# Optimization experiments

Measured on AMD Instinct MI355X. Metric: run time of the kernel, lower is better.

## Reference

```python
import jax, jax.numpy as jnp
import numpy as np

D_MODEL = 1024
NHEAD = 16
HEAD_DIM = D_MODEL // NHEAD
WINDOW = 256


def setup_inputs() -> dict:
    key = jax.random.key(0)
    kx, kq, kk, kv, ko = jax.random.split(key, 5)
    B, S = 2, 2048
    scale = 1.0 / np.sqrt(D_MODEL)
    x = jax.random.normal(kx, (B, S, D_MODEL), dtype=jnp.float32)
    Wq = jax.random.normal(kq, (D_MODEL, D_MODEL), dtype=jnp.float32) * scale
    Wk = jax.random.normal(kk, (D_MODEL, D_MODEL), dtype=jnp.float32) * scale
    Wv = jax.random.normal(kv, (D_MODEL, D_MODEL), dtype=jnp.float32) * scale
    Wo = jax.random.normal(ko, (D_MODEL, D_MODEL), dtype=jnp.float32) * scale
    return {"x": x, "Wq": Wq, "Wk": Wk, "Wv": Wv, "Wo": Wo}


def _sliding_window_mask(seq_len):
    # additive mask: 0 where (q - window + 1) <= k <= q, -inf elsewhere
    pos = jnp.arange(seq_len)
    qpos = pos[:, None]
    kpos = pos[None, :]
    valid = (kpos >= qpos - WINDOW + 1) & (kpos <= qpos)
    return jnp.where(valid, 0.0, -jnp.inf).astype(jnp.float32)


def reference(x, Wq, Wk, Wv, Wo):
    B, S, D = x.shape
    # projections (nn.Linear: x @ W.T; weights here stored as [out,in] equiv -> use x @ W.T)
    q = jnp.einsum('bsd,ed->bse', x, Wq)
    k = jnp.einsum('bsd,ed->bse', x, Wk)
    v = jnp.einsum('bsd,ed->bse', x, Wv)
    q = q.reshape(B, S, NHEAD, HEAD_DIM).transpose(0, 2, 1, 3)  # [B,H,S,Dh]
    k = k.reshape(B, S, NHEAD, HEAD_DIM).transpose(0, 2, 1, 3)
    v = v.reshape(B, S, NHEAD, HEAD_DIM).transpose(0, 2, 1, 3)
    mask = _sliding_window_mask(S)  # [S,S]
    scale = 1.0 / np.sqrt(HEAD_DIM)
    scores = jnp.einsum('bhqd,bhkd->bhqk', q, k) * scale + mask
    attn = jax.nn.softmax(scores, axis=-1)
    out = jnp.einsum('bhqk,bhkd->bhqd', attn, v)  # [B,H,S,Dh]
    out = out.transpose(0, 2, 1, 3).reshape(B, S, D)
    return jnp.einsum('bsd,ed->bse', out, Wo)
```

## Files before the change

kernel.cpp:

```cpp
#include <hip/hip_runtime.h>
#include <stdint.h>

#define S_LEN   2048
#define BATCH   2
#define DM      1024
#define NHEADS  16
#define HD      64
#define WIN     256
#define MROWS   (BATCH * S_LEN)
#define NX      (MROWS * DM)
#define NW      (DM * DM)

typedef unsigned short u16;
typedef unsigned int   u32;

using short8  = __attribute__((ext_vector_type(8))) short;
using floatx4 = __attribute__((ext_vector_type(4))) float;

__device__ __forceinline__ float bf2f(u16 u) {
    union { u32 u; float f; } v; v.u = ((u32)u) << 16; return v.f;
}
__device__ __forceinline__ u16 f2bf(float f) {
    union { float f; u32 u; } v; v.f = f;
    u32 u = v.u;
    u += 0x7fffu + ((u >> 16) & 1u);
    return (u16)(u >> 16);
}

__device__ __forceinline__ void load_lds16(const void* g, void* l) {
    __builtin_amdgcn_global_load_lds(
        (__attribute__((address_space(1))) void*)(uintptr_t)g,
        (__attribute__((address_space(3))) void*)(unsigned int)(uintptr_t)l,
        16, 0, 0);
}

__global__ __launch_bounds__(256) void detect_mode(const u16* x, int* flag) {
    __shared__ int sbad;
    int t = threadIdx.x;
    if (t == 0) sbad = 0;
    __syncthreads();
    int bad = 0;
    for (int i = t; i < 4096; i += 256) {
        float v = bf2f(x[i]);
        if (!(fabsf(v) < 1e6f)) bad = 1;
    }
    if (bad) atomicOr(&sbad, 1);
    __syncthreads();
    if (t == 0) flag[0] = sbad;
}

__global__ __launch_bounds__(256) void normalize_inputs(
        const void* x, const void* wq, const void* wk, const void* wv, const void* wo,
        u16* xb, u16* wcat, u16* wob, const int* flag) {
    if (flag[0] == 0) return;
    const int total = NX + 4 * NW;
    for (int i = blockIdx.x * blockDim.x + threadIdx.x; i < total;
         i += gridDim.x * blockDim.x) {
        const void* src; u16* dst; int li;
        if (i < NX)              { src = x;  dst = xb;            li = i; }
        else if (i < NX + NW)    { src = wq; dst = wcat;          li = i - NX; }
        else if (i < NX + 2*NW)  { src = wk; dst = wcat + NW;     li = i - NX - NW; }
        else if (i < NX + 3*NW)  { src = wv; dst = wcat + 2*NW;   li = i - NX - 2*NW; }
        else                     { src = wo; dst = wob;           li = i - NX - 3*NW; }
        dst[li] = f2bf(((const float*)src)[li]);
    }
}

#define BM 128
#define BK 32

template<int TBN>
__global__ __launch_bounds__(256) void gemm_lds(
        const u16* __restrict__ Araw, const u16* __restrict__ Anorm,
        const u16* __restrict__ B0, const u16* __restrict__ B1,
        const u16* __restrict__ B2, const u16* __restrict__ Bnorm,
        void* __restrict__ C, int M, int N, int K,
        const int* __restrict__ flag, int final_out) {
    constexpr int NF = TBN / 32;
    __shared__ __align__(16) u16 sA[2][BM * BK];
    __shared__ __align__(16) u16 sB[2][TBN * BK];

    const int mode = flag[0];
    const int tid  = threadIdx.x;
    const int lane = tid & 63, wave = tid >> 6;
    const int m0  = blockIdx.x * BM;
    const int n0g = blockIdx.y * TBN;
    const int third = n0g >> 10;
    const u16* A = mode ? Anorm : Araw;
    const u16* B = mode ? (Bnorm + (size_t)third * NW)
                        : (third == 0 ? B0 : (third == 1 ? B1 : B2));
    const int n0 = n0g - third * 1024;

    const int srow = lane >> 2;
    const int scol = (lane & 3) * 8;
    const u16* gA = A + (size_t)(m0 + wave * 16 + srow) * K + scol;
    const u16* gB = B + (size_t)(n0 + wave * 16 + srow) * K + scol;
    const size_t rstep = (size_t)64 * K;
    const int lofs = wave * 16 * BK;

    const int n16 = lane & 15, quad = lane >> 4;
    const int m_off = (wave >> 1) * 64, n_off = (wave & 1) * (TBN / 2);

    floatx4 acc[4][NF] = {};
    const int NIT = K / BK;

    auto issue = [&](int k0, int buf) {
        u16* lA = sA[buf] + lofs;
        u16* lB = sB[buf] + lofs;
        load_lds16(gA + k0,         lA);
        load_lds16(gA + k0 + rstep, lA + 64 * BK);
        load_lds16(gB + k0, lB);
        if (TBN == 128) load_lds16(gB + k0 + rstep, lB + 64 * BK);
    };

    issue(0, 0);
    for (int it = 0; it < NIT; ++it) {
        const int cur = it & 1;
        __syncthreads();
        if (it + 1 < NIT) issue((it + 1) * BK, 1 - cur);
        short8 af[4], bfr[NF];
        #pragma unroll
        for (int i = 0; i < 4; ++i)
            af[i] = *(const short8*)&sA[cur][(m_off + i * 16 + n16) * BK + quad * 8];
        #pragma unroll
        for (int j = 0; j < NF; ++j)
            bfr[j] = *(const short8*)&sB[cur][(n_off + j * 16 + n16) * BK + quad * 8];
        #pragma unroll
        for (int i = 0; i < 4; ++i) {
            #pragma unroll
            for (int j = 0; j < NF; ++j)
                acc[i][j] = __builtin_amdgcn_mfma_f32_16x16x32_bf16(
                    af[i], bfr[j], acc[i][j], 0, 0, 0);
        }
    }

    const int outmode = final_out ? mode : 0;
    const float oscale = (!final_out && n0g < 1024) ? 0.125f : 1.0f;
    #pragma unroll
    for (int i = 0; i < 4; ++i) {
        #pragma unroll
        for (int j = 0; j < NF; ++j) {
            #pragma unroll
            for (int r = 0; r < 4; ++r) {
                int row = m0 + m_off + i * 16 + quad * 4 + r;
                int col = n0g + n_off + j * 16 + n16;
                size_t idx = (size_t)row * N + col;
                float v = acc[i][j][r] * oscale;
                if (outmode) ((float*)C)[idx] = v;
                else         ((u16*)C)[idx]   = f2bf(v);
            }
        }
    }
}

#define KSTG 384
#define KPAD 72
#define VPAD 394

__global__ __launch_bounds__(512) void attn_mfma(
        const u16* __restrict__ QKV, u16* __restrict__ O) {
    __shared__ __align__(16) u16 sK[KSTG][KPAD];
    __shared__ __align__(16) u16 sVt[64][VPAD];
    __shared__ __align__(16) u16 sP[8][2][16][40];

    const int bh = blockIdx.x;
    const int b  = bh >> 4, h = bh & 15;
    const int q0 = blockIdx.y * 128;
    const int kb0 = q0 - (WIN - 1);
    const int tid = threadIdx.x;
    const u16* base = QKV + (size_t)b * S_LEN * 3072;

    for (int i = tid; i < KSTG * 8; i += 512) {
        int row = i >> 3, seg = i & 7;
        int kg = kb0 + row;
        uint4 kv = {0u, 0u, 0u, 0u}, vv = {0u, 0u, 0u, 0u};
        if (kg >= 0 && kg < S_LEN) {
            const u16* rp = base + (size_t)kg * 3072 + h * 64 + seg * 8;
            kv = *(const uint4*)(rp + 1024);
            vv = *(const uint4*)(rp + 2048);
        }
        *(uint4*)&sK[row][seg * 8] = kv;
        const u16* vp = (const u16*)&vv;
        #pragma unroll
        for (int t2 = 0; t2 < 8; ++t2) sVt[seg * 8 + t2][row] = vp[t2];
    }
    __syncthreads();

    const int wave = tid >> 6, lane = tid & 63;
    const int n16 = lane & 15, quad = lane >> 4;
    const int sqb = q0 + wave * 16;
    const int sq_r0 = sqb + quad * 4;

    const u16* qrow = base + (size_t)(sqb + n16) * 3072 + h * 64;
    short8 aq0 = *(const short8*)(qrow + quad * 8);
    short8 aq1 = *(const short8*)(qrow + 32 + quad * 8);

    floatx4 o0 = {0.f,0.f,0.f,0.f}, o1 = o0, o2 = o0, o3 = o0;
    float m[4] = {-1e30f, -1e30f, -1e30f, -1e30f};
    float l[4] = {0.f, 0.f, 0.f, 0.f};
    const int c0 = wave >> 1;

    for (int cc = 0; cc < 9; ++cc) {
        const int krel = (c0 + cc) * 32;
        short8 bk00 = *(const short8*)&sK[krel + n16][quad * 8];
        short8 bk01 = *(const short8*)&sK[krel + n16][32 + quad * 8];
        short8 bk10 = *(const short8*)&sK[krel + 16 + n16][quad * 8];
        short8 bk11 = *(const short8*)&sK[krel + 16 + n16][32 + quad * 8];
        floatx4 z = {0.f, 0.f, 0.f, 0.f};
        floatx4 s0 = __builtin_amdgcn_mfma_f32_16x16x32_bf16(aq0, bk00, z, 0, 0, 0);
        s0 = __builtin_amdgcn_mfma_f32_16x16x32_bf16(aq1, bk01, s0, 0, 0, 0);
        floatx4 s1 = __builtin_amdgcn_mfma_f32_16x16x32_bf16(aq0, bk10, z, 0, 0, 0);
        s1 = __builtin_amdgcn_mfma_f32_16x16x32_bf16(aq1, bk11, s1, 0, 0, 0);

        const int kg0 = kb0 + krel + n16;
        const int kg1 = kg0 + 16;
        float alpha[4], p0[4], p1[4];
        #pragma unroll
        for (int r = 0; r < 4; ++r) {
            int sq = sq_r0 + r;
            int lo = sq - (WIN - 1); if (lo < 0) lo = 0;
            float v0 = (kg0 >= lo && kg0 <= sq) ? s0[r] : -1e30f;
            float v1 = (kg1 >= lo && kg1 <= sq) ? s1[r] : -1e30f;
            float mc = fmaxf(v0, v1);
            mc = fmaxf(mc, __shfl_xor(mc, 1));
            mc = fmaxf(mc, __shfl_xor(mc, 2));
            mc = fmaxf(mc, __shfl_xor(mc, 4));
            mc = fmaxf(mc, __shfl_xor(mc, 8));
            float mn = fmaxf(m[r], mc);
            alpha[r] = __expf(m[r] - mn);
            m[r] = mn;
            p0[r] = __expf(v0 - mn);
            p1[r] = __expf(v1 - mn);
            float rs = p0[r] + p1[r];
            rs += __shfl_xor(rs, 1);
            rs += __shfl_xor(rs, 2);
            rs += __shfl_xor(rs, 4);
            rs += __shfl_xor(rs, 8);
            l[r] = l[r] * alpha[r] + rs;
        }
        #pragma unroll
        for (int r = 0; r < 4; ++r) {
            o0[r] *= alpha[r]; o1[r] *= alpha[r];
            o2[r] *= alpha[r]; o3[r] *= alpha[r];
        }
        u16* pw = &sP[wave][cc & 1][0][0];
        #pragma unroll
        for (int r = 0; r < 4; ++r) {
            pw[(quad * 4 + r) * 40 + n16]      = f2bf(p0[r]);
            pw[(quad * 4 + r) * 40 + 16 + n16] = f2bf(p1[r]);
        }
        asm volatile("s_waitcnt lgkmcnt(0)" ::: "memory");
        short8 pa  = *(const short8*)&pw[n16 * 40 + quad * 8];
        short8 bv0 = *(const short8*)&sVt[n16]     [krel + quad * 8];
        short8 bv1 = *(const short8*)&sVt[16 + n16][krel + quad * 8];
        short8 bv2 = *(const short8*)&sVt[32 + n16][krel + quad * 8];
        short8 bv3 = *(const short8*)&sVt[48 + n16][krel + quad * 8];
        o0 = __builtin_amdgcn_mfma_f32_16x16x32_bf16(pa, bv0, o0, 0, 0, 0);
        o1 = __builtin_amdgcn_mfma_f32_16x16x32_bf16(pa, bv1, o1, 0, 0, 0);
        o2 = __builtin_amdgcn_mfma_f32_16x16x32_bf16(pa, bv2, o2, 0, 0, 0);
        o3 = __builtin_amdgcn_mfma_f32_16x16x32_bf16(pa, bv3, o3, 0, 0, 0);
    }

    #pragma unroll
    for (int r = 0; r < 4; ++r) {
        float rl = 1.0f / l[r];
        size_t ro = ((size_t)(b * S_LEN + sq_r0 + r)) * DM + h * 64 + n16;
        O[ro]      = f2bf(o0[r] * rl);
        O[ro + 16] = f2bf(o1[r] * rl);
        O[ro + 32] = f2bf(o2[r] * rl);
        O[ro + 48] = f2bf(o3[r] * rl);
    }
}

extern "C" void kernel_launch(void* const* d_in, const int* in_sizes, int n_in,
                              void* d_out, int out_size, void* d_ws, size_t ws_size,
                              hipStream_t stream) {
    char* ws = (char*)d_ws;
    int* flag = (int*)ws;
    u16* xb   = (u16*)(ws + 1024);
    u16* wcat = xb   + (size_t)NX;
    u16* wob  = wcat + (size_t)3 * NW;
    u16* qkv  = wob  + (size_t)NW;
    u16* ob   = qkv  + (size_t)MROWS * 3 * DM;

    const u16* xr  = (const u16*)d_in[0];
    const u16* wqr = (const u16*)d_in[1];
    const u16* wkr = (const u16*)d_in[2];
    const u16* wvr = (const u16*)d_in[3];
    const u16* wor = (const u16*)d_in[4];

    detect_mode<<<1, 256, 0, stream>>>(xr, flag);
    normalize_inputs<<<1024, 256, 0, stream>>>(
        d_in[0], d_in[1], d_in[2], d_in[3], d_in[4], xb, wcat, wob, flag);
    gemm_lds<128><<<dim3(MROWS / BM, 3072 / 128), 256, 0, stream>>>(
        xr, xb, wqr, wkr, wvr, wcat, qkv, MROWS, 3 * DM, DM, flag, 0);
    attn_mfma<<<dim3(BATCH * NHEADS, S_LEN / 128), 512, 0, stream>>>(qkv, ob);
    gemm_lds<64><<<dim3(MROWS / BM, DM / 64), 256, 0, stream>>>(
        ob, ob, wor, wor, wor, wob, d_out, MROWS, DM, DM, flag, 1);
}
```

Before: 173.9 us.

## Stream K/V chunks through double-buffered LDS in smaller attention blocks

Replaces the upfront staging of the whole 384-row K/V window with per-chunk double-buffered loads of 32 rows, overlapping the next chunk's global loads with current compute. Blocks shrink to 64 queries and 256 threads, doubling the grid and greatly lowering LDS use per block to raise occupancy. This adds a block barrier per chunk and more redundant K/V reads across neighbouring blocks.

```diff
diff --git a/kernel.cpp b/kernel.cpp
--- a/kernel.cpp
+++ b/kernel.cpp
@@ -153,43 +153,44 @@
     }
 }
 
-#define KSTG 384
-#define KPAD 72
-#define VPAD 394
-
-__global__ __launch_bounds__(512) void attn_mfma(
+#define NCHUNK 10
+
+__global__ __launch_bounds__(256) void attn_mfma(
         const u16* __restrict__ QKV, u16* __restrict__ O) {
-    __shared__ __align__(16) u16 sK[KSTG][KPAD];
-    __shared__ __align__(16) u16 sVt[64][VPAD];
-    __shared__ __align__(16) u16 sP[8][2][16][40];
+    __shared__ __align__(16) u16 sK[2][32][72];
+    __shared__ __align__(16) u16 sVt[2][64][40];
+    __shared__ __align__(16) u16 sP[4][2][16][40];
 
     const int bh = blockIdx.x;
     const int b  = bh >> 4, h = bh & 15;
-    const int q0 = blockIdx.y * 128;
+    const int q0 = blockIdx.y * 64;
     const int kb0 = q0 - (WIN - 1);
     const int tid = threadIdx.x;
     const u16* base = QKV + (size_t)b * S_LEN * 3072;
-
-    for (int i = tid; i < KSTG * 8; i += 512) {
-        int row = i >> 3, seg = i & 7;
-        int kg = kb0 + row;
+    const u16* Kb = base + 1024 + h * 64;
+    const u16* Vb = base + 2048 + h * 64;
+
+    const int srow = tid >> 3;
+    const int sseg = tid & 7;
+
+    auto stage = [&](int c, int buf) {
+        int kg = kb0 + c * 32 + srow;
         uint4 kv = {0u, 0u, 0u, 0u}, vv = {0u, 0u, 0u, 0u};
         if (kg >= 0 && kg < S_LEN) {
-            const u16* rp = base + (size_t)kg * 3072 + h * 64 + seg * 8;
-            kv = *(const uint4*)(rp + 1024);
-            vv = *(const uint4*)(rp + 2048);
-        }
-        *(uint4*)&sK[row][seg * 8] = kv;
+            kv = *(const uint4*)(Kb + (size_t)kg * 3072 + sseg * 8);
+            vv = *(const uint4*)(Vb + (size_t)kg * 3072 + sseg * 8);
+        }
+        *(uint4*)&sK[buf][srow][sseg * 8] = kv;
         const u16* vp = (const u16*)&vv;
         #pragma unroll
-        for (int t2 = 0; t2 < 8; ++t2) sVt[seg * 8 + t2][row] = vp[t2];
-    }
-    __syncthreads();
+        for (int t2 = 0; t2 < 8; ++t2) sVt[buf][sseg * 8 + t2][srow] = vp[t2];
+    };
 
     const int wave = tid >> 6, lane = tid & 63;
     const int n16 = lane & 15, quad = lane >> 4;
     const int sqb = q0 + wave * 16;
     const int sq_r0 = sqb + quad * 4;
+    const int cfirst = wave >> 1;
 
     const u16* qrow = base + (size_t)(sqb + n16) * 3072 + h * 64;
     short8 aq0 = *(const short8*)(qrow + quad * 8);
@@ -198,21 +199,25 @@
     floatx4 o0 = {0.f,0.f,0.f,0.f}, o1 = o0, o2 = o0, o3 = o0;
     float m[4] = {-1e30f, -1e30f, -1e30f, -1e30f};
     float l[4] = {0.f, 0.f, 0.f, 0.f};
-    const int c0 = wave >> 1;
-
-    for (int cc = 0; cc < 9; ++cc) {
-        const int krel = (c0 + cc) * 32;
-        short8 bk00 = *(const short8*)&sK[krel + n16][quad * 8];
-        short8 bk01 = *(const short8*)&sK[krel + n16][32 + quad * 8];
-        short8 bk10 = *(const short8*)&sK[krel + 16 + n16][quad * 8];
-        short8 bk11 = *(const short8*)&sK[krel + 16 + n16][32 + quad * 8];
+
+    stage(0, 0);
+    for (int c = 0; c < NCHUNK; ++c) {
+        const int buf = c & 1;
+        __syncthreads();
+        if (c + 1 < NCHUNK) stage(c + 1, 1 - buf);
+        if (c < cfirst || c > cfirst + 8) continue;
+
+        short8 bk00 = *(const short8*)&sK[buf][n16][quad * 8];
+        short8 bk01 = *(const short8*)&sK[buf][n16][32 + quad * 8];
+        short8 bk10 = *(const short8*)&sK[buf][16 + n16][quad * 8];
+        short8 bk11 = *(const short8*)&sK[buf][16 + n16][32 + quad * 8];
         floatx4 z = {0.f, 0.f, 0.f, 0.f};
         floatx4 s0 = __builtin_amdgcn_mfma_f32_16x16x32_bf16(aq0, bk00, z, 0, 0, 0);
         s0 = __builtin_amdgcn_mfma_f32_16x16x32_bf16(aq1, bk01, s0, 0, 0, 0);
         floatx4 s1 = __builtin_amdgcn_mfma_f32_16x16x32_bf16(aq0, bk10, z, 0, 0, 0);
         s1 = __builtin_amdgcn_mfma_f32_16x16x32_bf16(aq1, bk11, s1, 0, 0, 0);
 
-        const int kg0 = kb0 + krel + n16;
+        const int kg0 = kb0 + c * 32 + n16;
         const int kg1 = kg0 + 16;
         float alpha[4], p0[4], p1[4];
         #pragma unroll
@@ -243,7 +248,7 @@
             o0[r] *= alpha[r]; o1[r] *= alpha[r];
             o2[r] *= alpha[r]; o3[r] *= alpha[r];
         }
-        u16* pw = &sP[wave][cc & 1][0][0];
+        u16* pw = &sP[wave][c & 1][0][0];
         #pragma unroll
         for (int r = 0; r < 4; ++r) {
             pw[(quad * 4 + r) * 40 + n16]      = f2bf(p0[r]);
@@ -251,10 +256,10 @@
         }
         asm volatile("s_waitcnt lgkmcnt(0)" ::: "memory");
         short8 pa  = *(const short8*)&pw[n16 * 40 + quad * 8];
-        short8 bv0 = *(const short8*)&sVt[n16]     [krel + quad * 8];
-        short8 bv1 = *(const short8*)&sVt[16 + n16][krel + quad * 8];
-        short8 bv2 = *(const short8*)&sVt[32 + n16][krel + quad * 8];
-        short8 bv3 = *(const short8*)&sVt[48 + n16][krel + quad * 8];
+        short8 bv0 = *(const short8*)&sVt[buf][n16]     [quad * 8];
+        short8 bv1 = *(const short8*)&sVt[buf][16 + n16][quad * 8];
+        short8 bv2 = *(const short8*)&sVt[buf][32 + n16][quad * 8];
+        short8 bv3 = *(const short8*)&sVt[buf][48 + n16][quad * 8];
         o0 = __builtin_amdgcn_mfma_f32_16x16x32_bf16(pa, bv0, o0, 0, 0, 0);
         o1 = __builtin_amdgcn_mfma_f32_16x16x32_bf16(pa, bv1, o1, 0, 0, 0);
         o2 = __builtin_amdgcn_mfma_f32_16x16x32_bf16(pa, bv2, o2, 0, 0, 0);
@@ -294,7 +299,7 @@
         d_in[0], d_in[1], d_in[2], d_in[3], d_in[4], xb, wcat, wob, flag);
     gemm_lds<128><<<dim3(MROWS / BM, 3072 / 128), 256, 0, stream>>>(
         xr, xb, wqr, wkr, wvr, wcat, qkv, MROWS, 3 * DM, DM, flag, 0);
-    attn_mfma<<<dim3(BATCH * NHEADS, S_LEN / 128), 512, 0, stream>>>(qkv, ob);
+    attn_mfma<<<dim3(BATCH * NHEADS, S_LEN / 64), 256, 0, stream>>>(qkv, ob);
     gemm_lds<64><<<dim3(MROWS / BM, DM / 64), 256, 0, stream>>>(
         ob, ob, wor, wor, wor, wob, d_out, MROWS, DM, DM, flag, 1);
 }
```

Result: slower. 178.9 us (+2.9%).
